# Kernel tuning notes

Measured on AMD Instinct MI355X. Metric: run time of the kernel, lower is better.

The kernel has to match this reference:

```python
import jax, jax.numpy as jnp
import numpy as np

HIDDEN = 1024
NUM_HEADS = 16
HEAD_DIM = HIDDEN // NUM_HEADS


def rotary_cos_sin(seq_len, head_dim, dtype=jnp.float32):
    inv_freq = 1.0 / (10000.0 ** (jnp.arange(0, head_dim, 2, dtype=dtype) / head_dim))
    t = jnp.arange(seq_len, dtype=dtype)
    freqs = jnp.einsum('i,j->ij', t, inv_freq)          # [S, hd/2]
    emb = jnp.concatenate([freqs, freqs], axis=-1)      # [S, hd]
    return jnp.cos(emb), jnp.sin(emb)


def apply_rotary(x, cos, sin):
    # x: [B, H, S, hd]; cos/sin: [S, hd]
    x1, x2 = jnp.split(x, 2, axis=-1)
    x_rot = jnp.concatenate([-x2, x1], axis=-1)
    return x * cos + x_rot * sin


def setup_inputs() -> dict:
    key = jax.random.key(0)
    ks = jax.random.split(key, 5)
    S, B = 2048, 2
    x = jax.random.normal(ks[0], (S, B, HIDDEN), dtype=jnp.float32)
    s = 1.0 / np.sqrt(HIDDEN)
    W_qkv = jax.random.uniform(ks[1], (HIDDEN, 3 * HIDDEN), jnp.float32, -s, s)
    b_qkv = jax.random.uniform(ks[2], (3 * HIDDEN,), jnp.float32, -s, s)
    W_out = jax.random.uniform(ks[3], (HIDDEN, HIDDEN), jnp.float32, -s, s)
    b_out = jax.random.uniform(ks[4], (HIDDEN,), jnp.float32, -s, s)
    return {"x": x, "W_qkv": W_qkv, "b_qkv": b_qkv, "W_out": W_out, "b_out": b_out}


def reference(x, W_qkv, b_qkv, W_out, b_out):
    S, B, D = x.shape
    scale = HEAD_DIM ** -0.5
    qkv = x @ W_qkv + b_qkv                               # [S, B, 3D]
    qkv = qkv.reshape(S, B, NUM_HEADS, 3 * HEAD_DIM)
    q, k, v = jnp.split(qkv, 3, axis=-1)                  # each [S, B, H, hd]
    q = q.transpose(1, 2, 0, 3)                           # [B, H, S, hd]
    k = k.transpose(1, 2, 0, 3)
    v = v.transpose(1, 2, 0, 3)
    cos, sin = rotary_cos_sin(S, HEAD_DIM, x.dtype)
    q = apply_rotary(q, cos, sin)
    k = apply_rotary(k, cos, sin)
    scores = jnp.einsum('bhqd,bhkd->bhqk', q, k) * scale  # [B, H, S, S]
    weights = jax.nn.softmax(scores, axis=-1)
    attn = jnp.einsum('bhqk,bhkd->bhqd', weights, v)      # [B, H, S, hd]
    attn = attn.transpose(2, 0, 1, 3).reshape(S, B, D)    # [S, B, D]
    return attn @ W_out + b_out
```

## Files before the change

### kernel.cpp

```cpp
#include <hip/hip_runtime.h>

typedef unsigned short u16;
typedef __attribute__((ext_vector_type(8))) short bf16x8;
typedef __attribute__((ext_vector_type(4))) float f32x4;
typedef __attribute__((ext_vector_type(16))) float f32x16;

#define S_LEN 2048
#define BATCH 2
#define HID 1024
#define NH 16
#define HD 64
#define MROWS 4096
#define QKV_N 3072
#define QSCALE 0.18033688011112042f

__device__ __forceinline__ u16 f2bf(float f) {
  unsigned u = __float_as_uint(f);
  u += 0x7fffu + ((u >> 16) & 1u);
  return (u16)(u >> 16);
}

__device__ __forceinline__ float bf2f(u16 u) {
  return __uint_as_float((unsigned)u << 16);
}

__device__ __forceinline__ float fexp2(float x) {
  float r; asm("v_exp_f32 %0, %1" : "=v"(r) : "v"(x)); return r;
}

__device__ __forceinline__ unsigned cvtpk(float lo, float hi) {
  unsigned r; asm("v_cvt_pk_bf16_f32 %0, %1, %2" : "=v"(r) : "v"(lo), "v"(hi)); return r;
}

__device__ __forceinline__ void gl2lds16(const u16* src, u16* lds) {
  __builtin_amdgcn_global_load_lds((__attribute__((address_space(1))) void*)(void*)src,
                                   (__attribute__((address_space(3))) void*)(void*)lds,
                                   16, 0, 0);
}

__device__ __forceinline__ void castT_body(const float* __restrict__ W, u16* __restrict__ Wt,
                                           int Ncols, int Krows, int bx, int by,
                                           float (*tile)[33]) {
  int c0 = bx * 32, r0 = by * 32;
  int tx = threadIdx.x & 31, ty = threadIdx.x >> 5;
  #pragma unroll
  for (int i = 0; i < 4; ++i)
    tile[ty + i * 8][tx] = W[(size_t)(r0 + ty + i * 8) * Ncols + c0 + tx];
  __syncthreads();
  #pragma unroll
  for (int i = 0; i < 4; ++i) {
    int a = ty + i * 8;
    Wt[(size_t)(c0 + a) * Krows + r0 + tx] = f2bf(tile[tx][a]);
  }
}

__global__ __launch_bounds__(256) void prep(
    const float* __restrict__ x, const float* __restrict__ W_qkv,
    const float* __restrict__ W_out, u16* __restrict__ xb,
    u16* __restrict__ Wqt, u16* __restrict__ Wot, float2* __restrict__ rope) {
  __shared__ float tile[32][33];
  const int bid = blockIdx.x;
  if (bid < 2048) {
    int i = bid * 256 + threadIdx.x;
    const float4* p = (const float4*)x;
    float4 a = p[2 * i], b = p[2 * i + 1];
    union { u16 us[8]; uint4 v; } o;
    o.us[0] = f2bf(a.x); o.us[1] = f2bf(a.y); o.us[2] = f2bf(a.z); o.us[3] = f2bf(a.w);
    o.us[4] = f2bf(b.x); o.us[5] = f2bf(b.y); o.us[6] = f2bf(b.z); o.us[7] = f2bf(b.w);
    *(uint4*)&xb[8 * i] = o.v;
  } else if (bid < 2048 + 3072) {
    int r = bid - 2048;
    castT_body(W_qkv, Wqt, QKV_N, HID, r % 96, r / 96, tile);
  } else if (bid < 2048 + 3072 + 1024) {
    int r = bid - (2048 + 3072);
    castT_body(W_out, Wot, HID, HID, r % 32, r / 32, tile);
  } else {
    int i = (bid - 6144) * 256 + threadIdx.x;
    int s = i >> 5, j = i & 31;
    float invf = fexp2(-(float)(2 * j) * (13.287712379549449f / 64.0f));
    float ang = (float)s * invf;
    rope[i] = make_float2(cosf(ang), sinf(ang));
  }
}

__global__ __launch_bounds__(256, 2) void gemm_qkv(
    const u16* __restrict__ A, const u16* __restrict__ Bt,
    const float* __restrict__ bias, const float2* __restrict__ rope,
    u16* __restrict__ Qb, u16* __restrict__ Kb, u16* __restrict__ VtOut) {
  __shared__ u16 As[128 * 32];
  __shared__ u16 Bs[128 * 32];
  __shared__ u16 vt[2][64][64];
  const int tid = threadIdx.x;
  const int lane = tid & 63, wid = tid >> 6;
  const int g = lane >> 4, l15 = lane & 15;
  const int bm0 = blockIdx.x * 128, bn0 = blockIdx.y * 128;
  const int wm = wid >> 1, wn = wid & 1;

  f32x4 acc[4][4] = {};
  for (int kt = 0; kt < 32; ++kt) {
    const int k0 = kt * 32;
    __syncthreads();
    #pragma unroll
    for (int it = 0; it < 2; ++it) {
      int s = it * 256 + tid;
      gl2lds16(A  + (size_t)(bm0 + (s >> 2)) * 1024 + k0 + (s & 3) * 8, &As[s * 8]);
      gl2lds16(Bt + (size_t)(bn0 + (s >> 2)) * 1024 + k0 + (s & 3) * 8, &Bs[s * 8]);
    }
    __syncthreads();
    bf16x8 af[4], bfr[4];
    #pragma unroll
    for (int m = 0; m < 4; ++m) af[m]  = *(const bf16x8*)&As[(wm * 64 + m * 16 + l15) * 32 + g * 8];
    #pragma unroll
    for (int n = 0; n < 4; ++n) bfr[n] = *(const bf16x8*)&Bs[(wn * 64 + n * 16 + l15) * 32 + g * 8];
    #pragma unroll
    for (int m = 0; m < 4; ++m)
      #pragma unroll
      for (int n = 0; n < 4; ++n)
        acc[m][n] = __builtin_amdgcn_mfma_f32_16x16x32_bf16(af[m], bfr[n], acc[m][n], 0, 0, 0);
  }

  const int cw0 = bn0 + wn * 64;
  const int gi = cw0 >> 6;
  const int h = gi / 3, tt = gi % 3;
  float bs[4];
  #pragma unroll
  for (int n = 0; n < 4; ++n) bs[n] = bias[cw0 + n * 16 + l15];
  const size_t hb = (size_t)h * (S_LEN * HD);

  if (tt == 2) {
    #pragma unroll
    for (int m = 0; m < 4; ++m)
      #pragma unroll
      for (int reg = 0; reg < 4; ++reg) {
        int rl = wm * 64 + m * 16 + g * 4 + reg;
        int srow = rl >> 1, b = reg & 1;
        #pragma unroll
        for (int n = 0; n < 4; ++n) {
          int d = n * 16 + l15;
          vt[b][d][srow ^ ((d & 7) << 3)] = f2bf(acc[m][n][reg] + bs[n]);
        }
      }
  } else {
    u16* dst = (tt == 0) ? Qb : Kb;
    const float scl = (tt == 0) ? QSCALE : 1.0f;
    #pragma unroll
    for (int m = 0; m < 4; ++m)
      #pragma unroll
      for (int reg = 0; reg < 4; ++reg) {
        int r = bm0 + wm * 64 + m * 16 + g * 4 + reg;
        int srow = r >> 1, b = r & 1;
        size_t o = (size_t)(b * NH) * (S_LEN * HD) + hb + (size_t)srow * HD;
        #pragma unroll
        for (int n = 0; n < 2; ++n) {
          int dlo = n * 16 + l15;
          float2 cs = rope[srow * 32 + dlo];
          float v1 = acc[m][n][reg] + bs[n];
          float v2 = acc[m][n + 2][reg] + bs[n + 2];
          dst[o + dlo]      = f2bf((v1 * cs.x - v2 * cs.y) * scl);
          dst[o + dlo + 32] = f2bf((v2 * cs.x + v1 * cs.y) * scl);
        }
      }
  }
  __syncthreads();
  if (tt == 2) {
    const int vtid = wm * 64 + lane;
    const int s0g = bm0 >> 1;
    #pragma unroll
    for (int it = 0; it < 8; ++it) {
      int task = vtid + it * 128;
      int b = task >> 9, d = (task >> 3) & 63, ch = task & 7;
      uint4 v = *(const uint4*)&vt[b][d][(ch ^ (d & 7)) * 8];
      *(uint4*)&VtOut[((size_t)(b * NH + h) * HD + d) * S_LEN + s0g + ch * 8] = v;
    }
  }
}

__global__ __launch_bounds__(256, 4) void attn_fwd(
    const u16* __restrict__ Qb, const u16* __restrict__ Kb,
    const u16* __restrict__ Vt, u16* __restrict__ part0,
    u16* __restrict__ part1, float2* __restrict__ stats) {
  __shared__ u16 Ks[2][64 * 64];
  __shared__ u16 Vs[2][64 * 64];
  const int tid = threadIdx.x;
  const int lane = tid & 63, wid = tid >> 6;
  const int l31 = lane & 31, h = lane >> 5;
  const int pp = blockIdx.x & 63;
  const int bh = pp >> 1, split = pp & 1;
  const int kt0 = split * 16;
  const int qw0 = (blockIdx.x >> 6) * 128 + wid * 32;
  const u16* Qp = Qb + ((size_t)bh * S_LEN + qw0) * HD;
  const u16* Kp = Kb + (size_t)bh * S_LEN * HD;
  const u16* Vp = Vt + (size_t)bh * HD * S_LEN;

  const int sA = tid, sB = tid + 256;
  const int srA = sA >> 3, srB = sB >> 3;
  const int sswA = (sA & 7) ^ (srA & 7), sswB = (sB & 7) ^ (srB & 7);
  #define SIGMA(sr) (((sr >> 4) & 1) * 16 + ((sr >> 2) & 1) * 8 \
                   + (((sr) & 3) | (((sr >> 3) & 1) << 2)) + ((sr) >> 5) * 32)
  const u16* kgA = Kp + (size_t)SIGMA(srA) * HD + sswA * 8;
  const u16* kgB = Kp + (size_t)SIGMA(srB) * HD + sswB * 8;
  const u16* vgA = Vp + (size_t)srA * S_LEN + sswA * 8;
  const u16* vgB = Vp + (size_t)srB * S_LEN + sswB * 8;
  #undef SIGMA

  bf16x8 qf0 = *(const bf16x8*)&Qp[(size_t)l31 * HD +  0 + h * 8];
  bf16x8 qf1 = *(const bf16x8*)&Qp[(size_t)l31 * HD + 16 + h * 8];
  bf16x8 qf2 = *(const bf16x8*)&Qp[(size_t)l31 * HD + 32 + h * 8];
  bf16x8 qf3 = *(const bf16x8*)&Qp[(size_t)l31 * HD + 48 + h * 8];

  f32x16 po0 = {}, po1 = {};
  float mrun = -INFINITY, lrun = 0.f;

  gl2lds16(kgA + (size_t)kt0 * 64 * HD, &Ks[0][sA * 8]);
  gl2lds16(kgB + (size_t)kt0 * 64 * HD, &Ks[0][sB * 8]);
  gl2lds16(vgA + kt0 * 64, &Vs[0][sA * 8]);
  gl2lds16(vgB + kt0 * 64, &Vs[0][sB * 8]);
  __syncthreads();

  for (int i = 0; i < 16; ++i) {
    const int bb = i & 1;
    if (i + 1 < 16) {
      const size_t ko = (size_t)(kt0 + i + 1) * 64 * HD;
      const int vo = (kt0 + i + 1) * 64;
      gl2lds16(kgA + ko, &Ks[bb ^ 1][sA * 8]);
      gl2lds16(kgB + ko, &Ks[bb ^ 1][sB * 8]);
      gl2lds16(vgA + vo, &Vs[bb ^ 1][sA * 8]);
      gl2lds16(vgB + vo, &Vs[bb ^ 1][sB * 8]);
    }
    const u16* KsB = Ks[bb];
    const u16* VsB = Vs[bb];

    f32x16 s0 = {}, s1 = {};
    __builtin_amdgcn_s_setprio(1);
    #pragma unroll
    for (int s = 0; s < 4; ++s) {
      const bf16x8 qf = (s == 0) ? qf0 : (s == 1) ? qf1 : (s == 2) ? qf2 : qf3;
      const int csw = ((2 * s + h) ^ (l31 & 7)) * 8;
      bf16x8 kf0 = *(const bf16x8*)&KsB[l31 * 64 + csw];
      s0 = __builtin_amdgcn_mfma_f32_32x32x16_bf16(kf0, qf, s0, 0, 0, 0);
      bf16x8 kf1 = *(const bf16x8*)&KsB[(32 + l31) * 64 + csw];
      s1 = __builtin_amdgcn_mfma_f32_32x32x16_bf16(kf1, qf, s1, 0, 0, 0);
    }
    __builtin_amdgcn_s_setprio(0);

    float tm = -INFINITY;
    #pragma unroll
    for (int r = 0; r < 16; ++r) tm = fmaxf(tm, fmaxf(s0[r], s1[r]));
    tm = fmaxf(tm, __shfl_xor(tm, 32));

    if (!__all(tm <= mrun + 8.f)) {
      float mnew = fmaxf(mrun, tm);
      float alpha = fexp2(mrun - mnew);
      mrun = mnew;
      lrun *= alpha;
      #pragma unroll
      for (int r = 0; r < 16; ++r) {
        float ar = __shfl(alpha, (r & 3) + 8 * (r >> 2) + 4 * h);
        po0[r] *= ar;
        po1[r] *= ar;
      }
    }

    float rs = 0.f;
    unsigned pwa[8], pwb[8];
    #pragma unroll
    for (int w = 0; w < 8; ++w) {
      float a = fexp2(s0[2 * w] - mrun), b = fexp2(s0[2 * w + 1] - mrun);
      rs += a + b;
      pwa[w] = cvtpk(a, b);
    }
    #pragma unroll
    for (int w = 0; w < 8; ++w) {
      float a = fexp2(s1[2 * w] - mrun), b = fexp2(s1[2 * w + 1] - mrun);
      rs += a + b;
      pwb[w] = cvtpk(a, b);
    }
    rs += __shfl_xor(rs, 32);
    lrun += rs;

    __builtin_amdgcn_s_setprio(1);
    #pragma unroll
    for (int s = 0; s < 4; ++s) {
      union { unsigned w[4]; bf16x8 v; } pf;
      if (s == 0)      { pf.w[0] = pwa[0]; pf.w[1] = pwa[1]; pf.w[2] = pwa[2]; pf.w[3] = pwa[3]; }
      else if (s == 1) { pf.w[0] = pwa[4]; pf.w[1] = pwa[5]; pf.w[2] = pwa[6]; pf.w[3] = pwa[7]; }
      else if (s == 2) { pf.w[0] = pwb[0]; pf.w[1] = pwb[1]; pf.w[2] = pwb[2]; pf.w[3] = pwb[3]; }
      else             { pf.w[0] = pwb[4]; pf.w[1] = pwb[5]; pf.w[2] = pwb[6]; pf.w[3] = pwb[7]; }
      const int csw = ((2 * s + h) ^ (l31 & 7)) * 8;
      bf16x8 vf0 = *(const bf16x8*)&VsB[l31 * 64 + csw];
      po0 = __builtin_amdgcn_mfma_f32_32x32x16_bf16(pf.v, vf0, po0, 0, 0, 0);
      bf16x8 vf1 = *(const bf16x8*)&VsB[(32 + l31) * 64 + csw];
      po1 = __builtin_amdgcn_mfma_f32_32x32x16_bf16(pf.v, vf1, po1, 0, 0, 0);
    }
    __builtin_amdgcn_s_setprio(0);
    __syncthreads();
  }

  u16* part = split ? part1 : part0;
  if (h == 0)
    stats[(size_t)split * (32 * 2048) + (size_t)bh * 2048 + qw0 + l31] =
        make_float2(mrun, lrun);
  #pragma unroll
  for (int r = 0; r < 16; ++r) {
    int q = qw0 + (r & 3) + 8 * (r >> 2) + 4 * h;
    size_t o = ((size_t)bh * 2048 + q) * 64 + l31;
    part[o]      = f2bf(po0[r]);
    part[o + 32] = f2bf(po1[r]);
  }
}

__global__ void attn_combine(const u16* __restrict__ part0, const u16* __restrict__ part1,
                             const float2* __restrict__ stats, u16* __restrict__ attn2d) {
  int t = blockIdx.x * 256 + threadIdx.x;
  int bh = t >> 14, r = t & 16383, q = r >> 3, dc = r & 7;
  int b = bh >> 4, h = bh & 15;
  float2 s0 = stats[bh * 2048 + q];
  float2 s1 = stats[32 * 2048 + bh * 2048 + q];
  float M = fmaxf(s0.x, s1.x);
  float w0 = fexp2(s0.x - M), w1 = fexp2(s1.x - M);
  float inv = 1.f / (w0 * s0.y + w1 * s1.y);
  w0 *= inv; w1 *= inv;
  size_t off = ((size_t)bh * 2048 + q) * 64 + dc * 8;
  union { uint4 v; u16 us[8]; } a, c, o;
  a.v = *(const uint4*)&part0[off];
  c.v = *(const uint4*)&part1[off];
  #pragma unroll
  for (int j = 0; j < 8; ++j)
    o.us[j] = f2bf(w0 * bf2f(a.us[j]) + w1 * bf2f(c.us[j]));
  *(uint4*)&attn2d[((size_t)q * BATCH + b) * HID + h * HD + dc * 8] = o.v;
}

__global__ __launch_bounds__(256, 4) void gemm_out(
    const u16* __restrict__ A, const u16* __restrict__ Bt,
    const float* __restrict__ bias, float* __restrict__ out) {
  __shared__ u16 As[64 * 32];
  __shared__ u16 Bs[64 * 32];
  const int tid = threadIdx.x;
  const int lane = tid & 63, wid = tid >> 6;
  const int g = lane >> 4, l15 = lane & 15;
  const int bm0 = blockIdx.x * 64, bn0 = blockIdx.y * 64;

  f32x4 acc[4] = {};
  for (int kt = 0; kt < 32; ++kt) {
    const int k0 = kt * 32;
    __syncthreads();
    gl2lds16(A  + (size_t)(bm0 + (tid >> 2)) * 1024 + k0 + (tid & 3) * 8, &As[tid * 8]);
    gl2lds16(Bt + (size_t)(bn0 + (tid >> 2)) * 1024 + k0 + (tid & 3) * 8, &Bs[tid * 8]);
    __syncthreads();
    bf16x8 af = *(const bf16x8*)&As[(wid * 16 + l15) * 32 + g * 8];
    bf16x8 bfr[4];
    #pragma unroll
    for (int n = 0; n < 4; ++n) bfr[n] = *(const bf16x8*)&Bs[(n * 16 + l15) * 32 + g * 8];
    #pragma unroll
    for (int n = 0; n < 4; ++n)
      acc[n] = __builtin_amdgcn_mfma_f32_16x16x32_bf16(af, bfr[n], acc[n], 0, 0, 0);
  }
  #pragma unroll
  for (int n = 0; n < 4; ++n) {
    int c = bn0 + n * 16 + l15;
    float bv = bias[c];
    #pragma unroll
    for (int reg = 0; reg < 4; ++reg) {
      int r = bm0 + wid * 16 + g * 4 + reg;
      out[(size_t)r * HID + c] = acc[n][reg] + bv;
    }
  }
}

extern "C" void kernel_launch(void* const* d_in, const int* in_sizes, int n_in,
                              void* d_out, int out_size, void* d_ws, size_t ws_size,
                              hipStream_t stream) {
  const float* x     = (const float*)d_in[0];
  const float* W_qkv = (const float*)d_in[1];
  const float* b_qkv = (const float*)d_in[2];
  const float* W_out = (const float*)d_in[3];
  const float* b_out = (const float*)d_in[4];
  float* out = (float*)d_out;

  char* ws = (char*)d_ws;
  size_t off = 0;
  auto carve = [&](size_t bytes) { void* p = ws + off; off += (bytes + 255) & ~(size_t)255; return p; };
  u16* xb      = (u16*)carve((size_t)MROWS * HID * 2);
  u16* Wqt     = (u16*)carve((size_t)QKV_N * HID * 2);
  u16* Wot     = (u16*)carve((size_t)HID * HID * 2);
  float2* rope = (float2*)carve((size_t)S_LEN * 32 * 8);
  u16* Qb      = (u16*)carve((size_t)BATCH * NH * S_LEN * HD * 2);
  u16* Kb      = (u16*)carve((size_t)BATCH * NH * S_LEN * HD * 2);
  u16* part1   = (u16*)carve((size_t)BATCH * NH * S_LEN * HD * 2);
  u16* Vt      = (u16*)carve((size_t)BATCH * NH * S_LEN * HD * 2);
  u16* attn2d  = (u16*)carve((size_t)MROWS * HID * 2);
  float2* stats= (float2*)carve((size_t)2 * 32 * 2048 * 8);

  prep<<<6400, 256, 0, stream>>>(x, W_qkv, W_out, xb, Wqt, Wot, rope);
  gemm_qkv<<<dim3(MROWS / 128, QKV_N / 128), 256, 0, stream>>>(xb, Wqt, b_qkv, rope, Qb, Kb, Vt);
  attn_fwd<<<1024, 256, 0, stream>>>(Qb, Kb, Vt, xb, part1, stats);
  attn_combine<<<2048, 256, 0, stream>>>(xb, part1, stats, attn2d);
  gemm_out<<<dim3(MROWS / 64, HID / 64), 256, 0, stream>>>(attn2d, Wot, b_out, out);
}
```

Measured before the change: 124.6 us.

## Fuse split-KV attention combine into attn_fwd via intra-block LDS reduction

The two KV splits of each query tile now run as two 256-thread halves of a single 512-thread block instead of separate blocks. After the main loop, the second half writes its fp32 partial output and softmax stats to shared memory, and the first half merges them and writes attn2d directly. This removes the attn_combine launch and the global round-trip of bf16 partials and stats. In exchange, blocks are larger with 64KB of LDS each, which may limit occupancy, and the whole tile now waits on a block-wide barrier before the epilogue.

```diff
diff --git a/kernel.cpp b/kernel.cpp
--- a/kernel.cpp
+++ b/kernel.cpp
@@ -175,24 +175,25 @@
   }
 }
 
-__global__ __launch_bounds__(256, 4) void attn_fwd(
+__global__ __launch_bounds__(512, 4) void attn_fwd(
     const u16* __restrict__ Qb, const u16* __restrict__ Kb,
-    const u16* __restrict__ Vt, u16* __restrict__ part0,
-    u16* __restrict__ part1, float2* __restrict__ stats) {
-  __shared__ u16 Ks[2][64 * 64];
-  __shared__ u16 Vs[2][64 * 64];
+    const u16* __restrict__ Vt, u16* __restrict__ attn2d) {
+  __shared__ u16 smem[32768];
   const int tid = threadIdx.x;
   const int lane = tid & 63, wid = tid >> 6;
   const int l31 = lane & 31, h = lane >> 5;
-  const int pp = blockIdx.x & 63;
-  const int bh = pp >> 1, split = pp & 1;
-  const int kt0 = split * 16;
-  const int qw0 = (blockIdx.x >> 6) * 128 + wid * 32;
+  const int sg = tid >> 8;
+  const int wid4 = wid & 3;
+  const int bh = blockIdx.x & 31;
+  const int b = bh >> 4, head = bh & 15;
+  const int kt0 = sg * 16;
+  const int qw0 = (blockIdx.x >> 5) * 128 + wid4 * 32;
   const u16* Qp = Qb + ((size_t)bh * S_LEN + qw0) * HD;
   const u16* Kp = Kb + (size_t)bh * S_LEN * HD;
   const u16* Vp = Vt + (size_t)bh * HD * S_LEN;
 
-  const int sA = tid, sB = tid + 256;
+  const int t8 = tid & 255;
+  const int sA = t8, sB = t8 + 256;
   const int srA = sA >> 3, srB = sB >> 3;
   const int sswA = (sA & 7) ^ (srA & 7), sswB = (sB & 7) ^ (srB & 7);
   #define SIGMA(sr) (((sr >> 4) & 1) * 16 + ((sr >> 2) & 1) * 8 \
@@ -202,6 +203,8 @@
   const u16* vgA = Vp + (size_t)srA * S_LEN + sswA * 8;
   const u16* vgB = Vp + (size_t)srB * S_LEN + sswB * 8;
   #undef SIGMA
+  u16* Kst[2] = { &smem[(sg * 2 + 0) * 4096], &smem[(sg * 2 + 1) * 4096] };
+  u16* Vst[2] = { &smem[16384 + (sg * 2 + 0) * 4096], &smem[16384 + (sg * 2 + 1) * 4096] };
 
   bf16x8 qf0 = *(const bf16x8*)&Qp[(size_t)l31 * HD +  0 + h * 8];
   bf16x8 qf1 = *(const bf16x8*)&Qp[(size_t)l31 * HD + 16 + h * 8];
@@ -211,10 +214,10 @@
   f32x16 po0 = {}, po1 = {};
   float mrun = -INFINITY, lrun = 0.f;
 
-  gl2lds16(kgA + (size_t)kt0 * 64 * HD, &Ks[0][sA * 8]);
-  gl2lds16(kgB + (size_t)kt0 * 64 * HD, &Ks[0][sB * 8]);
-  gl2lds16(vgA + kt0 * 64, &Vs[0][sA * 8]);
-  gl2lds16(vgB + kt0 * 64, &Vs[0][sB * 8]);
+  gl2lds16(kgA + (size_t)kt0 * 64 * HD, &Kst[0][sA * 8]);
+  gl2lds16(kgB + (size_t)kt0 * 64 * HD, &Kst[0][sB * 8]);
+  gl2lds16(vgA + kt0 * 64, &Vst[0][sA * 8]);
+  gl2lds16(vgB + kt0 * 64, &Vst[0][sB * 8]);
   __syncthreads();
 
   for (int i = 0; i < 16; ++i) {
@@ -222,13 +225,13 @@
     if (i + 1 < 16) {
       const size_t ko = (size_t)(kt0 + i + 1) * 64 * HD;
       const int vo = (kt0 + i + 1) * 64;
-      gl2lds16(kgA + ko, &Ks[bb ^ 1][sA * 8]);
-      gl2lds16(kgB + ko, &Ks[bb ^ 1][sB * 8]);
-      gl2lds16(vgA + vo, &Vs[bb ^ 1][sA * 8]);
-      gl2lds16(vgB + vo, &Vs[bb ^ 1][sB * 8]);
-    }
-    const u16* KsB = Ks[bb];
-    const u16* VsB = Vs[bb];
+      gl2lds16(kgA + ko, &Kst[bb ^ 1][sA * 8]);
+      gl2lds16(kgB + ko, &Kst[bb ^ 1][sB * 8]);
+      gl2lds16(vgA + vo, &Vst[bb ^ 1][sA * 8]);
+      gl2lds16(vgB + vo, &Vst[bb ^ 1][sB * 8]);
+    }
+    const u16* KsB = Kst[bb];
+    const u16* VsB = Vst[bb];
 
     f32x16 s0 = {}, s1 = {};
     __builtin_amdgcn_s_setprio(1);
@@ -265,15 +268,15 @@
     unsigned pwa[8], pwb[8];
     #pragma unroll
     for (int w = 0; w < 8; ++w) {
-      float a = fexp2(s0[2 * w] - mrun), b = fexp2(s0[2 * w + 1] - mrun);
-      rs += a + b;
-      pwa[w] = cvtpk(a, b);
+      float a = fexp2(s0[2 * w] - mrun), bq = fexp2(s0[2 * w + 1] - mrun);
+      rs += a + bq;
+      pwa[w] = cvtpk(a, bq);
     }
     #pragma unroll
     for (int w = 0; w < 8; ++w) {
-      float a = fexp2(s1[2 * w] - mrun), b = fexp2(s1[2 * w + 1] - mrun);
-      rs += a + b;
-      pwb[w] = cvtpk(a, b);
+      float a = fexp2(s1[2 * w] - mrun), bq = fexp2(s1[2 * w + 1] - mrun);
+      rs += a + bq;
+      pwb[w] = cvtpk(a, bq);
     }
     rs += __shfl_xor(rs, 32);
     lrun += rs;
@@ -296,38 +299,40 @@
     __syncthreads();
   }
 
-  u16* part = split ? part1 : part0;
-  if (h == 0)
-    stats[(size_t)split * (32 * 2048) + (size_t)bh * 2048 + qw0 + l31] =
-        make_float2(mrun, lrun);
-  #pragma unroll
-  for (int r = 0; r < 16; ++r) {
-    int q = qw0 + (r & 3) + 8 * (r >> 2) + 4 * h;
-    size_t o = ((size_t)bh * 2048 + q) * 64 + l31;
-    part[o]      = f2bf(po0[r]);
-    part[o + 32] = f2bf(po1[r]);
-  }
-}
-
-__global__ void attn_combine(const u16* __restrict__ part0, const u16* __restrict__ part1,
-                             const float2* __restrict__ stats, u16* __restrict__ attn2d) {
-  int t = blockIdx.x * 256 + threadIdx.x;
-  int bh = t >> 14, r = t & 16383, q = r >> 3, dc = r & 7;
-  int b = bh >> 4, h = bh & 15;
-  float2 s0 = stats[bh * 2048 + q];
-  float2 s1 = stats[32 * 2048 + bh * 2048 + q];
-  float M = fmaxf(s0.x, s1.x);
-  float w0 = fexp2(s0.x - M), w1 = fexp2(s1.x - M);
-  float inv = 1.f / (w0 * s0.y + w1 * s1.y);
-  w0 *= inv; w1 *= inv;
-  size_t off = ((size_t)bh * 2048 + q) * 64 + dc * 8;
-  union { uint4 v; u16 us[8]; } a, c, o;
-  a.v = *(const uint4*)&part0[off];
-  c.v = *(const uint4*)&part1[off];
-  #pragma unroll
-  for (int j = 0; j < 8; ++j)
-    o.us[j] = f2bf(w0 * bf2f(a.us[j]) + w1 * bf2f(c.us[j]));
-  *(uint4*)&attn2d[((size_t)q * BATCH + b) * HID + h * HD + dc * 8] = o.v;
+  float* pc = (float*)smem;
+  float* st = pc + 8192;
+  if (sg == 1) {
+    #pragma unroll
+    for (int r = 0; r < 16; ++r) {
+      int crow = (r & 3) + 8 * (r >> 2) + 4 * h;
+      pc[wid4 * 2048 + crow * 64 + l31]      = po0[r];
+      pc[wid4 * 2048 + crow * 64 + 32 + l31] = po1[r];
+    }
+    if (h == 0) {
+      st[wid4 * 64 + l31 * 2]     = mrun;
+      st[wid4 * 64 + l31 * 2 + 1] = lrun;
+    }
+  }
+  __syncthreads();
+  if (sg == 0) {
+    float m1 = st[wid4 * 64 + l31 * 2];
+    float l1 = st[wid4 * 64 + l31 * 2 + 1];
+    float M = fmaxf(mrun, m1);
+    float w0 = fexp2(mrun - M), w1 = fexp2(m1 - M);
+    float inv = 1.f / (w0 * lrun + w1 * l1);
+    w0 *= inv; w1 *= inv;
+    #pragma unroll
+    for (int r = 0; r < 16; ++r) {
+      int crow = (r & 3) + 8 * (r >> 2) + 4 * h;
+      float w0r = __shfl(w0, crow);
+      float w1r = __shfl(w1, crow);
+      float p1a = pc[wid4 * 2048 + crow * 64 + l31];
+      float p1b = pc[wid4 * 2048 + crow * 64 + 32 + l31];
+      size_t o = ((size_t)(qw0 + crow) * BATCH + b) * HID + head * HD + l31;
+      attn2d[o]      = f2bf(w0r * po0[r] + w1r * p1a);
+      attn2d[o + 32] = f2bf(w0r * po1[r] + w1r * p1b);
+    }
+  }
 }
 
 __global__ __launch_bounds__(256, 4) void gemm_out(
@@ -386,14 +391,11 @@
   float2* rope = (float2*)carve((size_t)S_LEN * 32 * 8);
   u16* Qb      = (u16*)carve((size_t)BATCH * NH * S_LEN * HD * 2);
   u16* Kb      = (u16*)carve((size_t)BATCH * NH * S_LEN * HD * 2);
-  u16* part1   = (u16*)carve((size_t)BATCH * NH * S_LEN * HD * 2);
   u16* Vt      = (u16*)carve((size_t)BATCH * NH * S_LEN * HD * 2);
-  u16* attn2d  = (u16*)carve((size_t)MROWS * HID * 2);
-  float2* stats= (float2*)carve((size_t)2 * 32 * 2048 * 8);
 
   prep<<<6400, 256, 0, stream>>>(x, W_qkv, W_out, xb, Wqt, Wot, rope);
   gemm_qkv<<<dim3(MROWS / 128, QKV_N / 128), 256, 0, stream>>>(xb, Wqt, b_qkv, rope, Qb, Kb, Vt);
-  attn_fwd<<<1024, 256, 0, stream>>>(Qb, Kb, Vt, xb, part1, stats);
-  attn_combine<<<2048, 256, 0, stream>>>(xb, part1, stats, attn2d);
+  u16* attn2d = xb;
+  attn_fwd<<<512, 512, 0, stream>>>(Qb, Kb, Vt, attn2d);
   gemm_out<<<dim3(MROWS / 64, HID / 64), 256, 0, stream>>>(attn2d, Wot, b_out, out);
 }
```

New measurement: 125.5 us. Within noise of the previous version (+0.7%).

## Fuse split-KV attention combine into output projection GEMM A-tile load

Applied to the files above, without the earlier changes.

Removes the separate attn_combine kernel and its attn2d intermediate. The output GEMM now reads both partial attention outputs and their softmax stats, merges them in registers while staging the A tile, and writes the result to LDS. This saves one launch and a round trip of the combined activation through global memory. In exchange, the combine work (stats loads, exp2, division) is repeated by each of the 16 column blocks of the GEMM, and the A loads become synchronous register loads instead of direct global-to-LDS copies.

```diff
diff --git a/kernel.cpp b/kernel.cpp
--- a/kernel.cpp
+++ b/kernel.cpp
@@ -265,15 +265,15 @@
     unsigned pwa[8], pwb[8];
     #pragma unroll
     for (int w = 0; w < 8; ++w) {
-      float a = fexp2(s0[2 * w] - mrun), b = fexp2(s0[2 * w + 1] - mrun);
-      rs += a + b;
-      pwa[w] = cvtpk(a, b);
+      float a = fexp2(s0[2 * w] - mrun), bq = fexp2(s0[2 * w + 1] - mrun);
+      rs += a + bq;
+      pwa[w] = cvtpk(a, bq);
     }
     #pragma unroll
     for (int w = 0; w < 8; ++w) {
-      float a = fexp2(s1[2 * w] - mrun), b = fexp2(s1[2 * w + 1] - mrun);
-      rs += a + b;
-      pwb[w] = cvtpk(a, b);
+      float a = fexp2(s1[2 * w] - mrun), bq = fexp2(s1[2 * w + 1] - mrun);
+      rs += a + bq;
+      pwb[w] = cvtpk(a, bq);
     }
     rs += __shfl_xor(rs, 32);
     lrun += rs;
@@ -309,29 +309,9 @@
   }
 }
 
-__global__ void attn_combine(const u16* __restrict__ part0, const u16* __restrict__ part1,
-                             const float2* __restrict__ stats, u16* __restrict__ attn2d) {
-  int t = blockIdx.x * 256 + threadIdx.x;
-  int bh = t >> 14, r = t & 16383, q = r >> 3, dc = r & 7;
-  int b = bh >> 4, h = bh & 15;
-  float2 s0 = stats[bh * 2048 + q];
-  float2 s1 = stats[32 * 2048 + bh * 2048 + q];
-  float M = fmaxf(s0.x, s1.x);
-  float w0 = fexp2(s0.x - M), w1 = fexp2(s1.x - M);
-  float inv = 1.f / (w0 * s0.y + w1 * s1.y);
-  w0 *= inv; w1 *= inv;
-  size_t off = ((size_t)bh * 2048 + q) * 64 + dc * 8;
-  union { uint4 v; u16 us[8]; } a, c, o;
-  a.v = *(const uint4*)&part0[off];
-  c.v = *(const uint4*)&part1[off];
-  #pragma unroll
-  for (int j = 0; j < 8; ++j)
-    o.us[j] = f2bf(w0 * bf2f(a.us[j]) + w1 * bf2f(c.us[j]));
-  *(uint4*)&attn2d[((size_t)q * BATCH + b) * HID + h * HD + dc * 8] = o.v;
-}
-
 __global__ __launch_bounds__(256, 4) void gemm_out(
-    const u16* __restrict__ A, const u16* __restrict__ Bt,
+    const u16* __restrict__ part0, const u16* __restrict__ part1,
+    const float2* __restrict__ stats, const u16* __restrict__ Bt,
     const float* __restrict__ bias, float* __restrict__ out) {
   __shared__ u16 As[64 * 32];
   __shared__ u16 Bs[64 * 32];
@@ -339,13 +319,32 @@
   const int lane = tid & 63, wid = tid >> 6;
   const int g = lane >> 4, l15 = lane & 15;
   const int bm0 = blockIdx.x * 64, bn0 = blockIdx.y * 64;
+  const int r = bm0 + (tid >> 2);
+  const int q = r >> 1, bb = r & 1;
+  const int ch = (tid & 3) * 8;
 
   f32x4 acc[4] = {};
   for (int kt = 0; kt < 32; ++kt) {
     const int k0 = kt * 32;
-    __syncthreads();
-    gl2lds16(A  + (size_t)(bm0 + (tid >> 2)) * 1024 + k0 + (tid & 3) * 8, &As[tid * 8]);
-    gl2lds16(Bt + (size_t)(bn0 + (tid >> 2)) * 1024 + k0 + (tid & 3) * 8, &Bs[tid * 8]);
+    const int head = kt >> 1;
+    const int bh = bb * 16 + head;
+    float2 st0 = stats[bh * 2048 + q];
+    float2 st1 = stats[32 * 2048 + bh * 2048 + q];
+    float M = fmaxf(st0.x, st1.x);
+    float w0 = fexp2(st0.x - M), w1 = fexp2(st1.x - M);
+    float inv = 1.f / (w0 * st0.y + w1 * st1.y);
+    w0 *= inv; w1 *= inv;
+    size_t po = ((size_t)bh * 2048 + q) * 64 + (k0 & 32) + ch;
+    union { uint4 v; u16 us[8]; } a, c;
+    a.v = *(const uint4*)&part0[po];
+    c.v = *(const uint4*)&part1[po];
+    union { u16 us[8]; uint4 v; } o;
+    #pragma unroll
+    for (int j = 0; j < 8; ++j)
+      o.us[j] = f2bf(w0 * bf2f(a.us[j]) + w1 * bf2f(c.us[j]));
+    __syncthreads();
+    *(uint4*)&As[tid * 8] = o.v;
+    gl2lds16(Bt + (size_t)(bn0 + (tid >> 2)) * 1024 + k0 + ch, &Bs[tid * 8]);
     __syncthreads();
     bf16x8 af = *(const bf16x8*)&As[(wid * 16 + l15) * 32 + g * 8];
     bf16x8 bfr[4];
@@ -361,8 +360,8 @@
     float bv = bias[c];
     #pragma unroll
     for (int reg = 0; reg < 4; ++reg) {
-      int r = bm0 + wid * 16 + g * 4 + reg;
-      out[(size_t)r * HID + c] = acc[n][reg] + bv;
+      int rr = bm0 + wid * 16 + g * 4 + reg;
+      out[(size_t)rr * HID + c] = acc[n][reg] + bv;
     }
   }
 }
@@ -388,12 +387,10 @@
   u16* Kb      = (u16*)carve((size_t)BATCH * NH * S_LEN * HD * 2);
   u16* part1   = (u16*)carve((size_t)BATCH * NH * S_LEN * HD * 2);
   u16* Vt      = (u16*)carve((size_t)BATCH * NH * S_LEN * HD * 2);
-  u16* attn2d  = (u16*)carve((size_t)MROWS * HID * 2);
   float2* stats= (float2*)carve((size_t)2 * 32 * 2048 * 8);
 
   prep<<<6400, 256, 0, stream>>>(x, W_qkv, W_out, xb, Wqt, Wot, rope);
   gemm_qkv<<<dim3(MROWS / 128, QKV_N / 128), 256, 0, stream>>>(xb, Wqt, b_qkv, rope, Qb, Kb, Vt);
   attn_fwd<<<1024, 256, 0, stream>>>(Qb, Kb, Vt, xb, part1, stats);
-  attn_combine<<<2048, 256, 0, stream>>>(xb, part1, stats, attn2d);
-  gemm_out<<<dim3(MROWS / 64, HID / 64), 256, 0, stream>>>(attn2d, Wot, b_out, out);
-}
+  gemm_out<<<dim3(MROWS / 64, HID / 64), 256, 0, stream>>>(xb, part1, stats, Wot, b_out, out);
+}
```

Result: slower. 137.1 us (+10.0%).
